# Kernel tuning notes

Measured on AMD Instinct MI355X. Metric: run time of the kernel, lower is better.

## Reference

```python
import jax, jax.numpy as jnp
import numpy as np

H = 8       # heads
D = 512     # hidden_size
DH = D // H # head dim
FF = 2048   # hardcoded FFN hidden in source


def _layernorm(x, g, b, eps=1e-5):
    mu = jnp.mean(x, axis=-1, keepdims=True)
    var = jnp.var(x, axis=-1, keepdims=True)
    return (x - mu) * jax.lax.rsqrt(var + eps) * g + b


def setup_inputs() -> dict:
    key = jax.random.key(0)
    ks = jax.random.split(key, 12)
    B, S = 2, 4096
    s = lambda fan_in: 1.0 / np.sqrt(fan_in)
    return {
        "reaction": jax.random.normal(ks[0], (B, S, D), dtype=jnp.float32),
        "mask": jnp.ones((B, 1, 1, S), dtype=jnp.int32),
        # attention weights stored as [in, out] (torch Linear weight.T)
        "Wq": jax.random.uniform(ks[1], (D, D), jnp.float32, -s(D), s(D)),
        "Wk": jax.random.uniform(ks[2], (D, D), jnp.float32, -s(D), s(D)),
        "Wv": jax.random.uniform(ks[3], (D, D), jnp.float32, -s(D), s(D)),
        "Wo": jax.random.uniform(ks[4], (D, D), jnp.float32, -s(D), s(D)),
        "bo": jnp.zeros((D,), jnp.float32),
        "W1": jax.random.uniform(ks[5], (D, FF), jnp.float32, -s(D), s(D)),
        "b1": jnp.zeros((FF,), jnp.float32),
        "W2": jax.random.uniform(ks[6], (FF, D), jnp.float32, -s(FF), s(FF)),
        "b2": jnp.zeros((D,), jnp.float32),
        "g_sa": jnp.ones((D,), jnp.float32),
        "b_sa": jnp.zeros((D,), jnp.float32),
        "g_ff": jnp.ones((D,), jnp.float32),
        "b_ff": jnp.zeros((D,), jnp.float32),
    }


def reference(reaction, mask, Wq, Wk, Wv, Wo, bo, W1, b1, W2, b2, g_sa, b_sa, g_ff, b_ff):
    B, S, _ = reaction.shape
    # --- self-attention part (pre-norm) ---
    x = _layernorm(reaction, g_sa, b_sa)
    q = (x @ Wq).reshape(B, S, H, DH)
    k = (x @ Wk).reshape(B, S, H, DH)
    v = (x @ Wv).reshape(B, S, H, DH)
    scale = DH ** (-0.5)
    scores = jnp.einsum('bqhd,bkhd->bhqk', q * scale, k)  # [B,H,S,S]
    scores = jnp.where(mask == 0, -jnp.inf, scores)
    att = jax.nn.softmax(scores, axis=-1)
    ctx = jnp.einsum('bhqk,bkhd->bqhd', att, v).reshape(B, S, D)
    attn_out = jax.nn.gelu(ctx @ Wo + bo, approximate=False)  # GELU after output proj (as in source)
    x = attn_out + reaction
    # --- feed-forward part (pre-norm) ---
    y = _layernorm(x, g_ff, b_ff)
    y = jax.nn.gelu(y @ W1 + b1, approximate=False) @ W2 + b2
    return y + x
```

## Files before the change

kernel.cpp:

```cpp
#include <hip/hip_runtime.h>
#include <hip/hip_bf16.h>
#include <math.h>

#define HN 8
#define DM 512
#define DHD 64
#define FFD 2048
#define BB 2
#define SS 4096
#define MT (BB*SS)

typedef __bf16 bf16_t;
typedef __bf16 bf16x8 __attribute__((ext_vector_type(8)));
typedef __bf16 bf16x4 __attribute__((ext_vector_type(4)));
typedef float  floatx4 __attribute__((ext_vector_type(4)));

__device__ __forceinline__ void async_copy16(const bf16_t* g, bf16_t* l) {
  __builtin_amdgcn_global_load_lds((const __attribute__((address_space(1))) void*)g,
                                   (__attribute__((address_space(3))) void*)l,
                                   16, 0, 0);
}

#if __has_builtin(__builtin_amdgcn_exp2f)
__device__ __forceinline__ float fast_exp2(float x) { return __builtin_amdgcn_exp2f(x); }
#else
__device__ __forceinline__ float fast_exp2(float x) { return __expf(x * 0.69314718056f); }
#endif

__device__ __forceinline__ float gelu_f(float x) {
  float y = 0.7978845608f * (x + 0.044715f * x * x * x);
  float e = fast_exp2(y * 2.885390082f);
  float th = 1.0f - 2.0f / (e + 1.0f);
  return 0.5f * x * (1.0f + th);
}

__global__ __launch_bounds__(256)
void prep_ln(const float* __restrict__ x, const float* __restrict__ g,
             const float* __restrict__ be, bf16_t* __restrict__ out,
             const float* __restrict__ Wq, const float* __restrict__ Wk,
             const float* __restrict__ Wv, const float* __restrict__ Wo,
             const float* __restrict__ W1, const float* __restrict__ W2,
             bf16_t* __restrict__ WqkvT, bf16_t* __restrict__ WoT,
             bf16_t* __restrict__ W1T, bf16_t* __restrict__ W2T)
{
  __shared__ float tile[32][33];
  if (blockIdx.x < 2048) {
    const int wave = threadIdx.x >> 6, lane = threadIdx.x & 63;
    const int row = blockIdx.x * 4 + wave;
    const float* xr = x + (size_t)row * DM + lane * 8;
    float4 a = *(const float4*)xr;
    float4 c = *(const float4*)(xr + 4);
    float s  = (a.x + a.y) + (a.z + a.w) + (c.x + c.y) + (c.z + c.w);
    float s2 = (a.x*a.x + a.y*a.y) + (a.z*a.z + a.w*a.w)
             + (c.x*c.x + c.y*c.y) + (c.z*c.z + c.w*c.w);
#pragma unroll
    for (int o = 1; o < 64; o <<= 1) { s += __shfl_xor(s, o); s2 += __shfl_xor(s2, o); }
    const float mu = s * (1.0f / DM);
    const float rv = rsqrtf(s2 * (1.0f / DM) - mu * mu + 1e-5f);
    float4 g0 = *(const float4*)(g + lane * 8);
    float4 g1 = *(const float4*)(g + lane * 8 + 4);
    float4 b0 = *(const float4*)(be + lane * 8);
    float4 b1 = *(const float4*)(be + lane * 8 + 4);
    bf16x8 o8;
    o8[0] = (bf16_t)((a.x - mu) * rv * g0.x + b0.x);
    o8[1] = (bf16_t)((a.y - mu) * rv * g0.y + b0.y);
    o8[2] = (bf16_t)((a.z - mu) * rv * g0.z + b0.z);
    o8[3] = (bf16_t)((a.w - mu) * rv * g0.w + b0.w);
    o8[4] = (bf16_t)((c.x - mu) * rv * g1.x + b1.x);
    o8[5] = (bf16_t)((c.y - mu) * rv * g1.y + b1.y);
    o8[6] = (bf16_t)((c.z - mu) * rv * g1.z + b1.z);
    o8[7] = (bf16_t)((c.w - mu) * rv * g1.w + b1.w);
    *(bf16x8*)(out + (size_t)row * DM + lane * 8) = o8;
    return;
  }
  const int bid = blockIdx.x - 2048;
  const float* src; bf16_t* dst; int Kd, Nd, n0, k0;
  if (bid < 768) {
    int seg = bid >> 8, t = bid & 255;
    src = (seg == 0) ? Wq : (seg == 1) ? Wk : Wv;
    dst = WqkvT + (size_t)seg * 512 * 512;
    Kd = 512; Nd = 512; n0 = (t & 15) * 32; k0 = (t >> 4) * 32;
  } else if (bid < 1024) {
    int t = bid - 768; src = Wo; dst = WoT;
    Kd = 512; Nd = 512; n0 = (t & 15) * 32; k0 = (t >> 4) * 32;
  } else if (bid < 2048) {
    int t = bid - 1024; src = W1; dst = W1T;
    Kd = 512; Nd = 2048; n0 = (t & 63) * 32; k0 = (t >> 6) * 32;
  } else {
    int t = bid - 2048; src = W2; dst = W2T;
    Kd = 2048; Nd = 512; n0 = (t & 15) * 32; k0 = (t >> 4) * 32;
  }
  const int tx4 = threadIdx.x & 7, tyr = threadIdx.x >> 3;
  float4 v4 = *(const float4*)(src + (size_t)(k0 + tyr) * Nd + n0 + tx4 * 4);
  tile[tyr][tx4 * 4 + 0] = v4.x;
  tile[tyr][tx4 * 4 + 1] = v4.y;
  tile[tyr][tx4 * 4 + 2] = v4.z;
  tile[tyr][tx4 * 4 + 3] = v4.w;
  __syncthreads();
  const int tx = threadIdx.x & 31, ty = threadIdx.x >> 5;
#pragma unroll
  for (int i = 0; i < 32; i += 8)
    dst[(size_t)(n0 + ty + i) * Kd + k0 + tx] = (bf16_t)tile[tx][ty + i];
}

__global__ __launch_bounds__(256)
void ln_kernel(const float* __restrict__ x, const float* __restrict__ g,
               const float* __restrict__ be, bf16_t* __restrict__ out)
{
  const int wave = threadIdx.x >> 6, lane = threadIdx.x & 63;
  const int row = blockIdx.x * 4 + wave;
  const float* xr = x + (size_t)row * DM + lane * 8;
  float4 a = *(const float4*)xr;
  float4 c = *(const float4*)(xr + 4);
  float s  = (a.x + a.y) + (a.z + a.w) + (c.x + c.y) + (c.z + c.w);
  float s2 = (a.x*a.x + a.y*a.y) + (a.z*a.z + a.w*a.w)
           + (c.x*c.x + c.y*c.y) + (c.z*c.z + c.w*c.w);
#pragma unroll
  for (int o = 1; o < 64; o <<= 1) { s += __shfl_xor(s, o); s2 += __shfl_xor(s2, o); }
  const float mu = s * (1.0f / DM);
  const float rv = rsqrtf(s2 * (1.0f / DM) - mu * mu + 1e-5f);
  float4 g0 = *(const float4*)(g + lane * 8);
  float4 g1 = *(const float4*)(g + lane * 8 + 4);
  float4 b0 = *(const float4*)(be + lane * 8);
  float4 b1 = *(const float4*)(be + lane * 8 + 4);
  bf16x8 o8;
  o8[0] = (bf16_t)((a.x - mu) * rv * g0.x + b0.x);
  o8[1] = (bf16_t)((a.y - mu) * rv * g0.y + b0.y);
  o8[2] = (bf16_t)((a.z - mu) * rv * g0.z + b0.z);
  o8[3] = (bf16_t)((a.w - mu) * rv * g0.w + b0.w);
  o8[4] = (bf16_t)((c.x - mu) * rv * g1.x + b1.x);
  o8[5] = (bf16_t)((c.y - mu) * rv * g1.y + b1.y);
  o8[6] = (bf16_t)((c.z - mu) * rv * g1.z + b1.z);
  o8[7] = (bf16_t)((c.w - mu) * rv * g1.w + b1.w);
  *(bf16x8*)(out + (size_t)row * DM + lane * 8) = o8;
}

template <int MI, int NJ, int EPI, int BKT = 64, int WV = 4>
__global__ __launch_bounds__(64 * WV)
void gemm_bt(const bf16_t* __restrict__ A, const bf16_t* __restrict__ Bt,
             const int M, const int N, const int K,
             const float* __restrict__ bias, const float* __restrict__ res,
             bf16_t* __restrict__ outb, float* __restrict__ outf,
             bf16_t* __restrict__ out2, bf16_t* __restrict__ out3, const int ldt)
{
  constexpr int THREADS = 64 * WV;
  constexpr int WN = WV / 2;
  constexpr int MTILE = 32 * MI, NTILE = 16 * NJ * WN;
  constexpr int CH = BKT / 8;
  constexpr int ACOPY = MTILE * BKT / (8 * THREADS);
  constexpr int BCOPY = NTILE * BKT / (8 * THREADS);
  __shared__ __align__(16) bf16_t lA[MTILE * BKT];
  __shared__ __align__(16) bf16_t lB[NTILE * BKT];
  const int tid = threadIdx.x;
  const int wave = tid >> 6, lane = tid & 63;
  const int wm = wave & 1, wn = wave >> 1;
  const int quad = lane >> 4, l16 = lane & 15;

  int srA[ACOPY > BCOPY ? ACOPY : BCOPY], scA[ACOPY > BCOPY ? ACOPY : BCOPY];
#pragma unroll
  for (int i = 0; i < (ACOPY > BCOPY ? ACOPY : BCOPY); ++i) {
    int flat = tid + THREADS * i;
    int r = flat / CH, ch = flat % CH;
    srA[i] = r;
    scA[i] = (ch ^ (r & (CH - 1))) * 8;
  }
  const bf16_t* Ab = A + (size_t)(blockIdx.x * MTILE) * K;
  const bf16_t* Bb = Bt + (size_t)(blockIdx.y * NTILE) * K;

  const floatx4 vzero = {0.f, 0.f, 0.f, 0.f};
  floatx4 acc[MI][NJ];
#pragma unroll
  for (int i = 0; i < MI; ++i)
#pragma unroll
    for (int j = 0; j < NJ; ++j) acc[i][j] = vzero;

  for (int k0 = 0; k0 < K; k0 += BKT) {
    __syncthreads();
#pragma unroll
    for (int i = 0; i < ACOPY; ++i)
      async_copy16(Ab + (size_t)srA[i] * K + k0 + scA[i], lA + (tid + THREADS * i) * 8);
#pragma unroll
    for (int i = 0; i < BCOPY; ++i)
      async_copy16(Bb + (size_t)srA[i] * K + k0 + scA[i], lB + (tid + THREADS * i) * 8);
    __syncthreads();
#pragma unroll
    for (int c = 0; c < BKT / 32; ++c) {
      bf16x8 af[MI], bfv[NJ];
#pragma unroll
      for (int i = 0; i < MI; ++i)
        af[i] = *(const bf16x8*)(lA + (wm * 16 * MI + i * 16 + l16) * BKT
                                 + (((c * 4 + quad) ^ (l16 & (CH - 1))) * 8));
#pragma unroll
      for (int j = 0; j < NJ; ++j)
        bfv[j] = *(const bf16x8*)(lB + (wn * 16 * NJ + j * 16 + l16) * BKT
                                  + (((c * 4 + quad) ^ (l16 & (CH - 1))) * 8));
#pragma unroll
      for (int i = 0; i < MI; ++i)
#pragma unroll
        for (int j = 0; j < NJ; ++j)
          acc[i][j] = __builtin_amdgcn_mfma_f32_16x16x32_bf16(af[i], bfv[j], acc[i][j], 0, 0, 0);
    }
  }

  const int m00 = blockIdx.x * MTILE + wm * 16 * MI;
  const int n00 = blockIdx.y * NTILE + wn * 16 * NJ;
#pragma unroll
  for (int i = 0; i < MI; ++i) {
#pragma unroll
    for (int j = 0; j < NJ; ++j) {
      const int m0 = m00 + i * 16 + quad * 4;
      const int n  = n00 + j * 16 + l16;
      floatx4 v = acc[i][j];
      if (EPI == 2) {
        const float bb = bias[n];
#pragma unroll
        for (int r = 0; r < 4; ++r)
          outf[(size_t)(m0 + r) * N + n] = gelu_f(v[r] + bb) + res[(size_t)(m0 + r) * N + n];
      } else if (EPI == 3) {
        const float bb = bias[n];
#pragma unroll
        for (int r = 0; r < 4; ++r)
          outb[(size_t)(m0 + r) * N + n] = (bf16_t)gelu_f(v[r] + bb);
      } else if (EPI == 4) {
        const float bb = bias[n];
#pragma unroll
        for (int r = 0; r < 4; ++r)
          outf[(size_t)(m0 + r) * N + n] = v[r] + bb + res[(size_t)(m0 + r) * N + n];
      } else {
        const int seg = blockIdx.y >> 2;
        if (seg == 0) {
#pragma unroll
          for (int r = 0; r < 4; ++r)
            outb[(size_t)(m0 + r) * 512 + n] = (bf16_t)(v[r] * 0.180336879f);
        } else if (seg == 1) {
#pragma unroll
          for (int r = 0; r < 4; ++r) out2[(size_t)(m0 + r) * 512 + (n - 512)] = (bf16_t)v[r];
        } else {
          const int o = m0 & 31;
          const int p0 = (m0 & ~31) + ((o >> 2) & 3) * 8 + ((o >> 4) << 2);
          bf16x4 pk = {(bf16_t)v[0], (bf16_t)v[1], (bf16_t)v[2], (bf16_t)v[3]};
          *(bf16x4*)(out3 + (size_t)(n - 1024) * ldt + p0) = pk;
        }
      }
    }
  }
}

__global__ __launch_bounds__(256, 2)
void attn_kernel(const bf16_t* __restrict__ qm, const bf16_t* __restrict__ km,
                 const bf16_t* __restrict__ vtm, const int* __restrict__ mask,
                 bf16_t* __restrict__ ctx)
{
  const int flat = blockIdx.x + 32 * (blockIdx.y + 8 * blockIdx.z);
  const int swz = (flat & 7) * 64 + (flat >> 3);
  const int b = swz >> 8, h = (swz >> 5) & 7;
  const int q0 = (swz & 31) * 128;
  const int tid = threadIdx.x;
  const int wave = tid >> 6, lane = tid & 63;
  const int quad = lane >> 4, l16 = lane & 15;

  __shared__ __align__(16) bf16_t lK[2][128 * DHD];
  __shared__ __align__(16) bf16_t lV[2][DHD * 128];
  __shared__ int sclean[4];

  const int* maskb = mask + b * SS;

  unsigned um = 0xFFFFFFFFu;
#pragma unroll
  for (int i = 0; i < 4; ++i) {
    int4 m = *(const int4*)(maskb + tid * 16 + i * 4);
    um = min(um, min(min((unsigned)m.x, (unsigned)m.y), min((unsigned)m.z, (unsigned)m.w)));
  }
#pragma unroll
  for (int o = 1; o < 64; o <<= 1) um = min(um, (unsigned)__shfl_xor((int)um, o));
  if (lane == 0) sclean[wave] = (int)um;
  __syncthreads();
  const bool clean = (min(min((unsigned)sclean[0], (unsigned)sclean[1]),
                          min((unsigned)sclean[2], (unsigned)sclean[3])) != 0u);

  const size_t qrow0 = (size_t)b * SS + q0;
  bf16x8 qa[2][2];
#pragma unroll
  for (int mb = 0; mb < 2; ++mb)
#pragma unroll
    for (int cc = 0; cc < 2; ++cc)
      qa[mb][cc] = *(const bf16x8*)(qm + (qrow0 + wave * 32 + mb * 16 + l16) * DM
                                    + h * DHD + cc * 32 + quad * 8);

  const floatx4 vzero = {0.f, 0.f, 0.f, 0.f};
  floatx4 cacc[2][4];
  float lsum[2] = {0.f, 0.f};
#pragma unroll
  for (int mb = 0; mb < 2; ++mb)
#pragma unroll
    for (int nb = 0; nb < 4; ++nb) cacc[mb][nb] = vzero;

  const bf16_t* Kb = km + (size_t)b * SS * DM + h * DHD;
  const bf16_t* Vb = vtm + (size_t)(h * DHD) * MT + (size_t)b * SS;

  const bf16_t* pk[4]; const bf16_t* pv[4];
#pragma unroll
  for (int i = 0; i < 4; ++i) {
    int p = tid + 256 * i;
    int key = p >> 3, cs = (p & 7) ^ (key & 7);
    pk[i] = Kb + (size_t)key * DM + cs * 8;
    int dh = p >> 4, cs2 = (p & 15) ^ (dh & 7);
    pv[i] = Vb + (size_t)dh * MT + cs2 * 8;
  }

  auto stage = [&](int buf, int s0) {
#pragma unroll
    for (int i = 0; i < 4; ++i) {
      int p8 = (tid + 256 * i) * 8;
      async_copy16(pk[i] + (size_t)s0 * DM, lK[buf] + p8);
      async_copy16(pv[i] + s0, lV[buf] + p8);
    }
  };

  auto exp_pv = [&](floatx4 sa[2], floatx4 sb[2], const bf16x8 av[4]) {
    bf16x8 pf[2];
#pragma unroll
    for (int mb = 0; mb < 2; ++mb) {
      float e0 = fast_exp2(sa[mb][0]), e1 = fast_exp2(sa[mb][1]);
      float e2 = fast_exp2(sa[mb][2]), e3 = fast_exp2(sa[mb][3]);
      float e4 = fast_exp2(sb[mb][0]), e5 = fast_exp2(sb[mb][1]);
      float e6 = fast_exp2(sb[mb][2]), e7 = fast_exp2(sb[mb][3]);
      lsum[mb] += ((e0 + e1) + (e2 + e3)) + ((e4 + e5) + (e6 + e7));
      pf[mb][0] = (bf16_t)e0; pf[mb][1] = (bf16_t)e1;
      pf[mb][2] = (bf16_t)e2; pf[mb][3] = (bf16_t)e3;
      pf[mb][4] = (bf16_t)e4; pf[mb][5] = (bf16_t)e5;
      pf[mb][6] = (bf16_t)e6; pf[mb][7] = (bf16_t)e7;
    }
    __builtin_amdgcn_s_setprio(1);
#pragma unroll
    for (int nb = 0; nb < 4; ++nb) {
      cacc[0][nb] = __builtin_amdgcn_mfma_f32_16x16x32_bf16(av[nb], pf[0], cacc[0][nb], 0, 0, 0);
      cacc[1][nb] = __builtin_amdgcn_mfma_f32_16x16x32_bf16(av[nb], pf[1], cacc[1][nb], 0, 0, 0);
    }
    __builtin_amdgcn_s_setprio(0);
  };

  if (clean) {
    auto compute_clean = [&](const bf16_t* __restrict__ lKb,
                             const bf16_t* __restrict__ lVb) {
      bf16x8 kf[2][2][2];
      bf16x8 av[2][4];
#pragma unroll
      for (int cc = 0; cc < 2; ++cc) {
        const int ko = ((cc * 4 + quad) ^ (l16 & 7)) * 8;
        kf[0][cc][0] = *(const bf16x8*)(lKb + (l16) * 64 + ko);
        kf[0][cc][1] = *(const bf16x8*)(lKb + (16 + l16) * 64 + ko);
      }
#pragma unroll
      for (int nb = 0; nb < 4; ++nb)
        av[0][nb] = *(const bf16x8*)(lVb + (nb * 16 + l16) * 128
                                     + ((quad ^ (l16 & 7)) * 8));
#pragma unroll
      for (int c = 0; c < 4; ++c) {
        const int buf = c & 1, nbuf = buf ^ 1;
        floatx4 sa[2], sb[2];
        sa[0] = vzero; sa[1] = vzero; sb[0] = vzero; sb[1] = vzero;
        __builtin_amdgcn_s_setprio(1);
#pragma unroll
        for (int cc = 0; cc < 2; ++cc)
#pragma unroll
          for (int mb = 0; mb < 2; ++mb) {
            sa[mb] = __builtin_amdgcn_mfma_f32_16x16x32_bf16(kf[buf][cc][0], qa[mb][cc], sa[mb], 0, 0, 0);
            sb[mb] = __builtin_amdgcn_mfma_f32_16x16x32_bf16(kf[buf][cc][1], qa[mb][cc], sb[mb], 0, 0, 0);
          }
        __builtin_amdgcn_s_setprio(0);
        if (c < 3) {
#pragma unroll
          for (int cc = 0; cc < 2; ++cc) {
            const int ko = (((cc * 4 + quad)) ^ (l16 & 7)) * 8;
            kf[nbuf][cc][0] = *(const bf16x8*)(lKb + ((c + 1) * 32 + l16) * 64 + ko);
            kf[nbuf][cc][1] = *(const bf16x8*)(lKb + ((c + 1) * 32 + 16 + l16) * 64 + ko);
          }
          const int chn = ((c + 1) * 4 + quad) ^ (l16 & 7);
#pragma unroll
          for (int nb = 0; nb < 4; ++nb)
            av[nbuf][nb] = *(const bf16x8*)(lVb + (nb * 16 + l16) * 128 + chn * 8);
        }
        exp_pv(sa, sb, av[buf]);
      }
    };

    stage(0, 0);
#pragma unroll 1
    for (int s0 = 0; s0 < SS; s0 += 256) {
      __syncthreads();
      stage(1, s0 + 128);
      compute_clean(lK[0], lV[0]);
      __syncthreads();
      if (s0 + 256 < SS) stage(0, s0 + 256);
      compute_clean(lK[1], lV[1]);
    }
  } else {
    auto compute_masked = [&](const bf16_t* __restrict__ lKb,
                              const bf16_t* __restrict__ lVb, int s0) {
#pragma unroll
      for (int c = 0; c < 4; ++c) {
        floatx4 sa[2], sb[2];
        sa[0] = vzero; sa[1] = vzero; sb[0] = vzero; sb[1] = vzero;
#pragma unroll
        for (int cc = 0; cc < 2; ++cc) {
          const int ko = ((cc * 4 + quad) ^ (l16 & 7)) * 8;
          bf16x8 kf0 = *(const bf16x8*)(lKb + (c * 32 + l16) * 64 + ko);
          bf16x8 kf1 = *(const bf16x8*)(lKb + (c * 32 + 16 + l16) * 64 + ko);
          __builtin_amdgcn_s_setprio(1);
#pragma unroll
          for (int mb = 0; mb < 2; ++mb) {
            sa[mb] = __builtin_amdgcn_mfma_f32_16x16x32_bf16(kf0, qa[mb][cc], sa[mb], 0, 0, 0);
            sb[mb] = __builtin_amdgcn_mfma_f32_16x16x32_bf16(kf1, qa[mb][cc], sb[mb], 0, 0, 0);
          }
          __builtin_amdgcn_s_setprio(0);
        }
        const int4 m0 = *(const int4*)(maskb + s0 + c * 32 + quad * 4);
        const int4 m1 = *(const int4*)(maskb + s0 + c * 32 + 16 + quad * 4);
#pragma unroll
        for (int mb = 0; mb < 2; ++mb) {
          if (m0.x == 0) sa[mb][0] = -1e30f;
          if (m0.y == 0) sa[mb][1] = -1e30f;
          if (m0.z == 0) sa[mb][2] = -1e30f;
          if (m0.w == 0) sa[mb][3] = -1e30f;
          if (m1.x == 0) sb[mb][0] = -1e30f;
          if (m1.y == 0) sb[mb][1] = -1e30f;
          if (m1.z == 0) sb[mb][2] = -1e30f;
          if (m1.w == 0) sb[mb][3] = -1e30f;
        }
        const int ch = (c * 4 + quad) ^ (l16 & 7);
        bf16x8 av[4];
#pragma unroll
        for (int nb = 0; nb < 4; ++nb)
          av[nb] = *(const bf16x8*)(lVb + (nb * 16 + l16) * 128 + ch * 8);
        exp_pv(sa, sb, av);
      }
    };

    stage(0, 0);
#pragma unroll 1
    for (int s0 = 0; s0 < SS; s0 += 256) {
      __syncthreads();
      stage(1, s0 + 128);
      compute_masked(lK[0], lV[0], s0);
      __syncthreads();
      if (s0 + 256 < SS) stage(0, s0 + 256);
      compute_masked(lK[1], lV[1], s0 + 128);
    }
  }

#pragma unroll
  for (int mb = 0; mb < 2; ++mb) {
    float tot = lsum[mb];
    tot += __shfl_xor(tot, 16);
    tot += __shfl_xor(tot, 32);
    const float inv = 1.0f / tot;
    const size_t qrow = qrow0 + wave * 32 + mb * 16 + l16;
#pragma unroll
    for (int nb = 0; nb < 4; ++nb) {
      bf16x4 o = {(bf16_t)(cacc[mb][nb][0] * inv), (bf16_t)(cacc[mb][nb][1] * inv),
                  (bf16_t)(cacc[mb][nb][2] * inv), (bf16_t)(cacc[mb][nb][3] * inv)};
      *(bf16x4*)(ctx + qrow * DM + h * DHD + nb * 16 + quad * 4) = o;
    }
  }
}

extern "C" void kernel_launch(void* const* d_in, const int* in_sizes, int n_in,
                              void* d_out, int out_size, void* d_ws, size_t ws_size,
                              hipStream_t stream)
{
  (void)in_sizes; (void)n_in; (void)out_size; (void)ws_size;
  const float* reaction = (const float*)d_in[0];
  const int*   mask     = (const int*)d_in[1];
  const float* Wq = (const float*)d_in[2];
  const float* Wk = (const float*)d_in[3];
  const float* Wv = (const float*)d_in[4];
  const float* Wo = (const float*)d_in[5];
  const float* bo = (const float*)d_in[6];
  const float* W1 = (const float*)d_in[7];
  const float* b1 = (const float*)d_in[8];
  const float* W2 = (const float*)d_in[9];
  const float* b2 = (const float*)d_in[10];
  const float* g_sa = (const float*)d_in[11];
  const float* b_sa = (const float*)d_in[12];
  const float* g_ff = (const float*)d_in[13];
  const float* b_ff = (const float*)d_in[14];
  float* out = (float*)d_out;

  char* ws = (char*)d_ws;
  size_t off = 0;
  auto take = [&](size_t bytes) -> char* {
    char* p = ws + off;
    off += (bytes + 255) & ~(size_t)255;
    return p;
  };

  bf16_t* xln   = (bf16_t*)take((size_t)MT * DM * 2);
  bf16_t* WqkvT = (bf16_t*)take((size_t)3 * DM * DM * 2);
  bf16_t* WoT   = (bf16_t*)take((size_t)DM * DM * 2);
  bf16_t* W1T   = (bf16_t*)take((size_t)FFD * DM * 2);
  bf16_t* W2T   = (bf16_t*)take((size_t)DM * FFD * 2);
  bf16_t* qb    = (bf16_t*)take((size_t)MT * DM * 2);
  bf16_t* kb    = (bf16_t*)take((size_t)MT * DM * 2);
  bf16_t* vtb   = (bf16_t*)take((size_t)DM * MT * 2);
  bf16_t* ctx   = (bf16_t*)take((size_t)MT * DM * 2);
  float*  x2    = (float*)take((size_t)MT * DM * 4);
  bf16_t* yb    = xln;
  bf16_t* hb    = qb;

  prep_ln<<<5120, 256, 0, stream>>>(reaction, g_sa, b_sa, xln,
                                    Wq, Wk, Wv, Wo, W1, W2, WqkvT, WoT, W1T, W2T);

  gemm_bt<4, 4, 5><<<dim3(64, 12), 256, 0, stream>>>(xln, WqkvT, MT, 3 * DM, DM,
                                                     nullptr, nullptr, qb, nullptr, kb, vtb, MT);

  attn_kernel<<<dim3(SS / 128, HN, BB), 256, 0, stream>>>(qb, kb, vtb, mask, ctx);

  gemm_bt<4, 2, 2, 128><<<dim3(64, 8), 256, 0, stream>>>(ctx, WoT, MT, DM, DM,
                                                         bo, reaction, nullptr, x2, nullptr, nullptr, 0);

  ln_kernel<<<MT / 4, 256, 0, stream>>>(x2, g_ff, b_ff, yb);
  gemm_bt<4, 4, 3, 64, 8><<<dim3(64, 8), 512, 0, stream>>>(yb, W1T, MT, FFD, DM,
                                                           b1, nullptr, hb, nullptr, nullptr, nullptr, 0);
  gemm_bt<4, 2, 4, 128><<<dim3(64, 8), 256, 0, stream>>>(hb, W2T, MT, DM, FFD,
                                                         b2, x2, nullptr, out, nullptr, nullptr, 0);
}
```

Measured before the change: 256.6 us.

## Add dedicated 256x256-tile FFN1 GEMM with phased async loads and MFMA interleave

Replaces the generic templated GEMM for the first FFN projection with a specialized kernel using 256x256 output tiles, 8 waves, and double-buffered LDS with XOR-swizzled layout. Each K-step is split into four phases that interleave LDS fragment reads, async global-to-LDS copies of the next tile, and MFMA bursts raised with s_setprio, aiming to overlap memory traffic with matrix math. The larger tile raises data reuse but uses 128 accumulator floats per thread and one block per CU, so only 256 blocks are launched, which risks lower occupancy and tail imbalance.

Result: slower. 261.8 us (+2.0%).

```diff
diff --git a/kernel.cpp b/kernel.cpp
--- a/kernel.cpp
+++ b/kernel.cpp
@@ -242,6 +242,138 @@
           *(bf16x4*)(out3 + (size_t)(n - 1024) * ldt + p0) = pk;
         }
       }
+    }
+  }
+}
+
+__global__ __launch_bounds__(512, 1)
+void gemm_ffn1_8ph(const bf16_t* __restrict__ A, const bf16_t* __restrict__ Bt,
+                   const float* __restrict__ bias, bf16_t* __restrict__ outb)
+{
+  constexpr int K = 512, N = FFD;
+  __shared__ __align__(16) bf16_t lA[2][256 * 64];
+  __shared__ __align__(16) bf16_t lB[2][256 * 64];
+  const int tid = threadIdx.x;
+  const int wave = tid >> 6, lane = tid & 63;
+  const int wm = wave & 1, wn = wave >> 1;
+  const int quad = lane >> 4, l16 = lane & 15;
+
+  int srow[4], scol[4];
+#pragma unroll
+  for (int i = 0; i < 4; ++i) {
+    int flat = tid + 512 * i;
+    srow[i] = flat >> 3;
+    scol[i] = ((flat & 7) ^ ((flat >> 3) & 7)) * 8;
+  }
+  const bf16_t* Ab = A + (size_t)(blockIdx.x * 256) * K;
+  const bf16_t* Bb = Bt + (size_t)(blockIdx.y * 256) * K;
+
+  const floatx4 vzero = {0.f, 0.f, 0.f, 0.f};
+  floatx4 acc[8][4];
+#pragma unroll
+  for (int i = 0; i < 8; ++i)
+#pragma unroll
+    for (int j = 0; j < 4; ++j) acc[i][j] = vzero;
+
+#pragma unroll
+  for (int i = 0; i < 4; ++i)
+    async_copy16(Ab + (size_t)srow[i] * K + scol[i], lA[0] + (tid + 512 * i) * 8);
+#pragma unroll
+  for (int i = 0; i < 4; ++i)
+    async_copy16(Bb + (size_t)srow[i] * K + scol[i], lB[0] + (tid + 512 * i) * 8);
+
+  const int rko = (l16 & 7);
+#pragma unroll 1
+  for (int t = 0; t < 8; ++t) {
+    const int buf = t & 1, nbuf = buf ^ 1;
+    const int nk = (t + 1) * 64;
+    bf16x8 bfr[4][2];
+    bf16x8 af[2][2];
+
+    if (t < 7) {
+#pragma unroll
+      for (int i = 0; i < 2; ++i)
+        async_copy16(Ab + (size_t)srow[i] * K + nk + scol[i], lA[nbuf] + (tid + 512 * i) * 8);
+      asm volatile("s_waitcnt vmcnt(2)" ::: "memory");
+    } else {
+      asm volatile("s_waitcnt vmcnt(0)" ::: "memory");
+    }
+    __builtin_amdgcn_s_barrier();
+    __builtin_amdgcn_sched_barrier(0);
+#pragma unroll
+    for (int j = 0; j < 4; ++j)
+#pragma unroll
+      for (int cc = 0; cc < 2; ++cc)
+        bfr[j][cc] = *(const bf16x8*)(lB[buf] + (wn * 64 + j * 16 + l16) * 64
+                                      + (((cc * 4 + quad) ^ rko) * 8));
+#pragma unroll
+    for (int r = 0; r < 2; ++r)
+#pragma unroll
+      for (int cc = 0; cc < 2; ++cc)
+        af[r][cc] = *(const bf16x8*)(lA[buf] + (wm * 128 + r * 16 + l16) * 64
+                                     + (((cc * 4 + quad) ^ rko) * 8));
+    __builtin_amdgcn_s_barrier();
+    __builtin_amdgcn_s_setprio(1);
+#pragma unroll
+    for (int cc = 0; cc < 2; ++cc)
+#pragma unroll
+      for (int r = 0; r < 2; ++r)
+#pragma unroll
+        for (int j = 0; j < 4; ++j)
+          acc[r][j] = __builtin_amdgcn_mfma_f32_16x16x32_bf16(af[r][cc], bfr[j][cc], acc[r][j], 0, 0, 0);
+    __builtin_amdgcn_s_setprio(0);
+
+#pragma unroll
+    for (int p = 1; p < 4; ++p) {
+#pragma unroll
+      for (int r = 0; r < 2; ++r)
+#pragma unroll
+        for (int cc = 0; cc < 2; ++cc)
+          af[r][cc] = *(const bf16x8*)(lA[buf] + (wm * 128 + (2 * p + r) * 16 + l16) * 64
+                                       + (((cc * 4 + quad) ^ rko) * 8));
+      if (t < 7) {
+        if (p == 1) {
+#pragma unroll
+          for (int i = 2; i < 4; ++i)
+            async_copy16(Ab + (size_t)srow[i] * K + nk + scol[i], lA[nbuf] + (tid + 512 * i) * 8);
+        } else if (p == 2) {
+#pragma unroll
+          for (int i = 0; i < 2; ++i)
+            async_copy16(Bb + (size_t)srow[i] * K + nk + scol[i], lB[nbuf] + (tid + 512 * i) * 8);
+        } else {
+#pragma unroll
+          for (int i = 2; i < 4; ++i)
+            async_copy16(Bb + (size_t)srow[i] * K + nk + scol[i], lB[nbuf] + (tid + 512 * i) * 8);
+        }
+      }
+      __builtin_amdgcn_s_barrier();
+      __builtin_amdgcn_s_setprio(1);
+#pragma unroll
+      for (int cc = 0; cc < 2; ++cc)
+#pragma unroll
+        for (int r = 0; r < 2; ++r)
+#pragma unroll
+          for (int j = 0; j < 4; ++j)
+            acc[2 * p + r][j] = __builtin_amdgcn_mfma_f32_16x16x32_bf16(af[r][cc], bfr[j][cc],
+                                                                        acc[2 * p + r][j], 0, 0, 0);
+      __builtin_amdgcn_s_setprio(0);
+    }
+    __builtin_amdgcn_s_barrier();
+  }
+
+  const int m00 = blockIdx.x * 256 + wm * 128;
+  const int n00 = blockIdx.y * 256 + wn * 64;
+#pragma unroll
+  for (int i = 0; i < 8; ++i) {
+#pragma unroll
+    for (int j = 0; j < 4; ++j) {
+      const int m0 = m00 + i * 16 + quad * 4;
+      const int n  = n00 + j * 16 + l16;
+      const float bb = bias[n];
+      floatx4 v = acc[i][j];
+#pragma unroll
+      for (int r = 0; r < 4; ++r)
+        outb[(size_t)(m0 + r) * N + n] = (bf16_t)gelu_f(v[r] + bb);
     }
   }
 }
@@ -520,8 +652,9 @@
                                                          bo, reaction, nullptr, x2, nullptr, nullptr, 0);
 
   ln_kernel<<<MT / 4, 256, 0, stream>>>(x2, g_ff, b_ff, yb);
-  gemm_bt<4, 4, 3, 64, 8><<<dim3(64, 8), 512, 0, stream>>>(yb, W1T, MT, FFD, DM,
-                                                           b1, nullptr, hb, nullptr, nullptr, nullptr, 0);
+
+  gemm_ffn1_8ph<<<dim3(32, 8), 512, 0, stream>>>(yb, W1T, b1, hb);
+
   gemm_bt<4, 2, 4, 128><<<dim3(64, 8), 256, 0, stream>>>(hb, W2T, MT, DM, FFD,
                                                          b2, x2, nullptr, out, nullptr, nullptr, 0);
 }
```
